# Performance work log

Measured on AMD Instinct MI355X. Metric: run time of the kernel, lower is better.

Reference implementation:

```python
import jax, jax.numpy as jnp
import numpy as np

B, L, D_MODEL, D_FF, N_EXPERTS, TOP_K = 32, 256, 512, 2048, 8, 2
EPS = 1e-9


def setup_inputs() -> dict:
    key = jax.random.key(0)
    ks = jax.random.split(key, 7)
    scale1 = 1.0 / np.sqrt(D_MODEL)
    scale2 = 1.0 / np.sqrt(D_FF)
    return {
        "cycle_curve_data": jax.random.normal(ks[0], (B, L, D_MODEL), jnp.float32),
        "logits": jax.random.normal(ks[1], (B, N_EXPERTS), jnp.float32),
        "moe_masks": jax.random.randint(ks[2], (B, N_EXPERTS), 0, 2, jnp.int32),
        "W1": jax.random.normal(ks[3], (N_EXPERTS, D_MODEL, D_FF), jnp.float32) * scale1,
        "b1": jax.random.normal(ks[4], (N_EXPERTS, D_FF), jnp.float32) * scale1,
        "W2": jax.random.normal(ks[5], (N_EXPERTS, D_FF, D_MODEL), jnp.float32) * scale2,
        "b2": jax.random.normal(ks[6], (N_EXPERTS, D_MODEL), jnp.float32) * scale2,
    }


def _gates(logits, moe_masks):
    # softmax over experts, zero out unavailable experts, keep top-k, renormalize
    mask = (moe_masks == 1).astype(logits.dtype)               # [B, E]
    p = jax.nn.softmax(logits, axis=1) * mask                  # [B, E]
    _, idx = jax.lax.top_k(p, TOP_K)                           # [B, K]
    topk_mask = jnp.zeros_like(p).at[jnp.arange(p.shape[0])[:, None], idx].set(1.0)
    p = p * topk_mask
    return p / (jnp.sum(p, axis=1, keepdims=True) + EPS)       # [B, E]


def reference(cycle_curve_data, logits, moe_masks, W1, b1, W2, b2):
    gates = _gates(logits, moe_masks)                          # [B, E]
    x = cycle_curve_data                                       # [B, L, D]
    # dense equivalent of per-expert gather -> MLP -> gate-weighted scatter-combine
    h = jnp.einsum("bld,edf->eblf", x, W1) + b1[:, None, None, :]   # [E,B,L,F]
    h = jax.nn.gelu(h, approximate=False)
    out = jnp.einsum("be,eblf,efd->bld", gates, h, W2)
    out = out + jnp.einsum("be,ed->bd", gates, b2)[:, None, :]      # [B,L,D]
    return out
```

## Files before the change

kernel.cpp:

```cpp
#include <hip/hip_runtime.h>

#define B_SZ 32
#define L_SZ 256
#define D_SZ 512
#define F_SZ 2048
#define E_SZ 8
#define P_SZ 64
#define BK2  32

typedef __attribute__((ext_vector_type(8)))  short bf16x8;
typedef __attribute__((ext_vector_type(16))) float f32x16;

__device__ __forceinline__ unsigned short f2bf(float f) {
  unsigned int u = __builtin_bit_cast(unsigned int, f);
  u += 0x7fffu + ((u >> 16) & 1u);
  return (unsigned short)(u >> 16);
}

__device__ __forceinline__ void async16(const void* g, void* l) {
  __builtin_amdgcn_global_load_lds(
      (const __attribute__((address_space(1))) unsigned int*)g,
      (__attribute__((address_space(3))) unsigned int*)l, 16, 0, 0);
}

__device__ __forceinline__ float gelu_f(float x) {
  float a = fabsf(x) * 0.70710678118654752f;
  float t = __builtin_amdgcn_rcpf(1.0f + 0.3275911f * a);
  float y = t * (0.254829592f +
            t * (-0.284496736f +
            t * (1.421413741f +
            t * (-1.453152027f +
            t * 1.061405429f))));
  float e = __expf(-a * a);
  float erf_abs = 1.0f - y * e;
  float erf_v = (x < 0.f) ? -erf_abs : erf_abs;
  return 0.5f * x * (1.0f + erf_v);
}

template <int NT>
__device__ __forceinline__ void transpose_tile(
    const float* __restrict__ ip, unsigned short* __restrict__ op,
    int R, int C, int r0, int c0, float* tile, int tid) {
  int tx = tid & 63, ty = tid >> 6;
  constexpr int RY = NT / 64;
#pragma unroll
  for (int i = 0; i < 64 / RY; ++i) {
    int r = i * RY + ty;
    tile[r * 65 + tx] = ip[(size_t)(r0 + r) * C + c0 + tx];
  }
  __syncthreads();
#pragma unroll
  for (int uu = 0; uu < 1024 / NT; ++uu) {
    int u = uu * NT + tid;
    int cc = u >> 4, q = u & 15;
    ushort4 o;
    o.x = f2bf(tile[(q * 4 + 0) * 65 + cc]);
    o.y = f2bf(tile[(q * 4 + 1) * 65 + cc]);
    o.z = f2bf(tile[(q * 4 + 2) * 65 + cc]);
    o.w = f2bf(tile[(q * 4 + 3) * 65 + cc]);
    *(ushort4*)(op + (size_t)(c0 + cc) * R + r0 + q * 4) = o;
  }
}

#define PREP_CONV_BLKS 4096
#define PREP_TR_BLKS   2048
#define PREP_TOTAL     (1 + PREP_CONV_BLKS + PREP_TR_BLKS)

__global__ __launch_bounds__(256) void prep_kernel(
    const float* __restrict__ logits, const int* __restrict__ masks,
    const float* __restrict__ x,
    const float* __restrict__ W1,
    int* __restrict__ sel_e, float* __restrict__ sel_g,
    unsigned short* __restrict__ xb,
    unsigned short* __restrict__ w1t) {
  __shared__ float tile[64 * 65];
  int blk = blockIdx.x;
  int tid = threadIdx.x;

  if (blk == 0) {
    int b = tid;
    if (b >= B_SZ) return;
    float lg[E_SZ], p[E_SZ];
    float mx = -1e30f;
    for (int e = 0; e < E_SZ; ++e) { lg[e] = logits[b * E_SZ + e]; mx = fmaxf(mx, lg[e]); }
    float s = 0.f;
    for (int e = 0; e < E_SZ; ++e) { p[e] = expf(lg[e] - mx); s += p[e]; }
    for (int e = 0; e < E_SZ; ++e) p[e] = (masks[b * E_SZ + e] == 1) ? (p[e] / s) : 0.f;
    int i0 = 0, i1 = 1; float v0 = -1.f, v1 = -1.f;
    for (int e = 0; e < E_SZ; ++e) {
      float v = p[e];
      if (v > v0)      { v1 = v0; i1 = i0; v0 = v; i0 = e; }
      else if (v > v1) { v1 = v;  i1 = e; }
    }
    float den = v0 + v1 + 1e-9f;
    sel_e[2 * b] = i0;  sel_e[2 * b + 1] = i1;
    sel_g[2 * b] = v0 / den;
    sel_g[2 * b + 1] = v1 / den;
    return;
  }
  blk -= 1;

  if (blk < PREP_CONV_BLKS) {
    int i = blk * 256 + tid;
    float4 v = ((const float4*)x)[i];
    ushort4 o;
    o.x = f2bf(v.x); o.y = f2bf(v.y); o.z = f2bf(v.z); o.w = f2bf(v.w);
    ((ushort4*)xb)[i] = o;
    return;
  }
  blk -= PREP_CONV_BLKS;

  int z = blk >> 8;
  int rem = blk & 255;
  int tr = rem >> 5, tc = rem & 31;
  transpose_tile<256>(W1 + (size_t)z * D_SZ * F_SZ, w1t + (size_t)z * D_SZ * F_SZ,
                      D_SZ, F_SZ, tr * 64, tc * 64, tile, tid);
}

__global__ __launch_bounds__(512, 4) void moe_gemm1(
    const unsigned short* __restrict__ Xb,
    const unsigned short* __restrict__ W1t,
    const float* __restrict__ b1,
    const int* __restrict__ sel_e,
    unsigned short* __restrict__ H,
    const float* __restrict__ W2,
    unsigned short* __restrict__ w2t) {
  __shared__ __align__(16) char smem[49152];
  int tid = threadIdx.x;
  int lin = blockIdx.x;

  if (lin >= 1024) {
    int blk = lin - 1024;
    int z = blk >> 8;
    int rem = blk & 255;
    int tr = rem >> 3, tc = rem & 7;
    transpose_tile<512>(W2 + (size_t)z * F_SZ * D_SZ, w2t + (size_t)z * F_SZ * D_SZ,
                        F_SZ, D_SZ, tr * 64, tc * 64, (float*)smem, tid);
    return;
  }

  unsigned short* As = (unsigned short*)smem;
  unsigned short* Bs = (unsigned short*)(smem + 16384);

  int f  = lin & 7;
  int l0 = ((lin >> 3) & 1) * 128;
  int p  = lin >> 4;
  int f0 = f * 256;
  int b  = p >> 1;
  int e  = sel_e[p];

  int lane = tid & 63;
  int w = tid >> 6;
  int wm = w & 1, wn = w >> 1;
  int m32 = lane & 31, kh = lane >> 5;
  int sw = (m32 >> 1) & 3;

  const unsigned short* Abase = Xb  + ((size_t)b * L_SZ + l0) * D_SZ;
  const unsigned short* Bbase = W1t + ((size_t)e * F_SZ + f0) * D_SZ;

  int sa   = tid;
  int rowa = sa >> 2,  ka  = ((sa  & 3) ^ ((rowa >> 1) & 3)) * 8;
  int sb1  = tid + 512;
  int rowb = sb1 >> 2, kb1 = ((sb1 & 3) ^ ((rowb >> 1) & 3)) * 8;

  const size_t aoffA  = (size_t)rowa * D_SZ + ka;
  const size_t aoffB1 = (size_t)rowb * D_SZ + kb1;

  f32x16 acc[2][2] = {};

#define G1_COMPUTE(CB)                                                       \
  _Pragma("unroll")                                                          \
  for (int s = 0; s < 2; ++s) {                                              \
    int ko = ((((s << 1) | kh) ^ sw) << 3);                                  \
    bf16x8 a0  = *(const bf16x8*)&As[(CB) * 4096 + (wm * 64 +      m32) * BK2 + ko]; \
    bf16x8 a1  = *(const bf16x8*)&As[(CB) * 4096 + (wm * 64 + 32 + m32) * BK2 + ko]; \
    bf16x8 b0  = *(const bf16x8*)&Bs[(CB) * 8192 + (wn * 64 +      m32) * BK2 + ko]; \
    bf16x8 b1f = *(const bf16x8*)&Bs[(CB) * 8192 + (wn * 64 + 32 + m32) * BK2 + ko]; \
    acc[0][0] = __builtin_amdgcn_mfma_f32_32x32x16_bf16(a0, b0,  acc[0][0], 0, 0, 0); \
    acc[0][1] = __builtin_amdgcn_mfma_f32_32x32x16_bf16(a0, b1f, acc[0][1], 0, 0, 0); \
    acc[1][0] = __builtin_amdgcn_mfma_f32_32x32x16_bf16(a1, b0,  acc[1][0], 0, 0, 0); \
    acc[1][1] = __builtin_amdgcn_mfma_f32_32x32x16_bf16(a1, b1f, acc[1][1], 0, 0, 0); \
  }

  async16(Abase + aoffA,  &As[sa * 8]);
  async16(Bbase + aoffA,  &Bs[sa * 8]);
  async16(Bbase + aoffB1, &Bs[sb1 * 8]);
  __syncthreads();

#pragma unroll 2
  for (int t = 0; t < 15; ++t) {
    int cb = t & 1, nb = cb ^ 1;
    int kk = (t + 1) * BK2;
    async16(Abase + aoffA  + kk, &As[nb * 4096 + sa * 8]);
    async16(Bbase + aoffA  + kk, &Bs[nb * 8192 + sa * 8]);
    async16(Bbase + aoffB1 + kk, &Bs[nb * 8192 + sb1 * 8]);
    G1_COMPUTE(cb)
    __syncthreads();
  }
  G1_COMPUTE(1)
#undef G1_COMPUTE

  float b1v[2];
#pragma unroll
  for (int tj = 0; tj < 2; ++tj)
    b1v[tj] = b1[e * F_SZ + f0 + wn * 64 + tj * 32 + m32];

  unsigned short* Hp = H + ((size_t)p * L_SZ + l0) * F_SZ + f0;
#pragma unroll
  for (int ti = 0; ti < 2; ++ti)
#pragma unroll
    for (int tj = 0; tj < 2; ++tj) {
      int col = wn * 64 + tj * 32 + m32;
#pragma unroll
      for (int r = 0; r < 16; ++r) {
        int row = wm * 64 + ti * 32 + (r & 3) + 8 * (r >> 2) + 4 * kh;
        Hp[(size_t)row * F_SZ + col] = f2bf(gelu_f(acc[ti][tj][r] + b1v[tj]));
      }
    }
}

__global__ __launch_bounds__(256, 4) void moe_gemm2(
    const unsigned short* __restrict__ H,
    const unsigned short* __restrict__ W2t,
    const float* __restrict__ b2,
    const int* __restrict__ sel_e,
    const float* __restrict__ sel_g,
    float* __restrict__ part,
    float* __restrict__ Out) {
  __shared__ __align__(16) unsigned short As[2][2][128 * BK2];
  __shared__ __align__(16) unsigned short Bs[2][2][128 * BK2];

  int lin = blockIdx.x;
  int q   = lin & 7;
  int d   = (lin >> 3) & 3;
  int g8  = lin >> 5;
  int gg  = g8 * 8 + q;
  int p   = gg >> 1;
  int l0  = (gg & 1) * 128;
  int d0  = d * 128;
  int b   = p >> 1;
  int e   = sel_e[p];
  float g = sel_g[p];

  int tid = threadIdx.x;
  int lane = tid & 63;
  int w = tid >> 6, wm = w & 1, wn = w >> 1;
  int m32 = lane & 31, kh = lane >> 5;
  int sw = (m32 >> 1) & 3;

  const unsigned short* Abase = H   + ((size_t)p * L_SZ + l0) * F_SZ;
  const unsigned short* Bbase = W2t + ((size_t)e * D_SZ + d0) * F_SZ;

  int seg0 = w * 128 + lane;
  int row0 = seg0 >> 2, ks0 = ((seg0 & 3) ^ ((row0 >> 1) & 3)) * 8;
  int seg1 = seg0 + 64;
  int row1 = seg1 >> 2, ks1 = ((seg1 & 3) ^ ((row1 >> 1) & 3)) * 8;

  const size_t aoff0 = (size_t)row0 * F_SZ + ks0;
  const size_t aoff1 = (size_t)row1 * F_SZ + ks1;

  f32x16 acc[2][2] = {};

#define G2_STAGE(NB, T) do {                                                 \
    size_t kk = (size_t)(T) * 64;                                            \
    async16(Abase + aoff0 + kk,      &As[NB][0][seg0 * 8]);                  \
    async16(Abase + aoff1 + kk,      &As[NB][0][seg1 * 8]);                  \
    async16(Bbase + aoff0 + kk,      &Bs[NB][0][seg0 * 8]);                  \
    async16(Bbase + aoff1 + kk,      &Bs[NB][0][seg1 * 8]);                  \
    async16(Abase + aoff0 + kk + 32, &As[NB][1][seg0 * 8]);                  \
    async16(Abase + aoff1 + kk + 32, &As[NB][1][seg1 * 8]);                  \
    async16(Bbase + aoff0 + kk + 32, &Bs[NB][1][seg0 * 8]);                  \
    async16(Bbase + aoff1 + kk + 32, &Bs[NB][1][seg1 * 8]);                  \
  } while (0)

#define G2_COMPUTE(CB)                                                       \
  _Pragma("unroll")                                                          \
  for (int h = 0; h < 2; ++h)                                                \
  _Pragma("unroll")                                                          \
  for (int s = 0; s < 2; ++s) {                                              \
    int ko = (((s << 1) | kh) ^ sw) << 3;                                    \
    bf16x8 a0  = *(const bf16x8*)&As[CB][h][(wm * 64 +      m32) * BK2 + ko]; \
    bf16x8 a1  = *(const bf16x8*)&As[CB][h][(wm * 64 + 32 + m32) * BK2 + ko]; \
    bf16x8 b0  = *(const bf16x8*)&Bs[CB][h][(wn * 64 +      m32) * BK2 + ko]; \
    bf16x8 b1f = *(const bf16x8*)&Bs[CB][h][(wn * 64 + 32 + m32) * BK2 + ko]; \
    acc[0][0] = __builtin_amdgcn_mfma_f32_32x32x16_bf16(a0, b0,  acc[0][0], 0, 0, 0); \
    acc[0][1] = __builtin_amdgcn_mfma_f32_32x32x16_bf16(a0, b1f, acc[0][1], 0, 0, 0); \
    acc[1][0] = __builtin_amdgcn_mfma_f32_32x32x16_bf16(a1, b0,  acc[1][0], 0, 0, 0); \
    acc[1][1] = __builtin_amdgcn_mfma_f32_32x32x16_bf16(a1, b1f, acc[1][1], 0, 0, 0); \
  }

  G2_STAGE(0, 0);
  __syncthreads();

#pragma unroll 2
  for (int t = 0; t < 31; ++t) {
    int cb = t & 1, nb = cb ^ 1;
    G2_STAGE(nb, t + 1);
    G2_COMPUTE(cb)
    __syncthreads();
  }
  G2_COMPUTE(1)
#undef G2_COMPUTE
#undef G2_STAGE

  float bias[2] = {0.f, 0.f};
  if (p & 1) {
    int e0 = sel_e[2 * b], e1 = sel_e[2 * b + 1];
    float g0 = sel_g[2 * b], g1 = sel_g[2 * b + 1];
#pragma unroll
    for (int tj = 0; tj < 2; ++tj) {
      int dd = d0 + wn * 64 + tj * 32 + m32;
      bias[tj] = g0 * b2[e0 * D_SZ + dd] + g1 * b2[e1 * D_SZ + dd];
    }
  }
  float* dst = (p & 1) ? Out : part;
  float* Op = dst + ((size_t)b * L_SZ + l0) * D_SZ + d0;
#pragma unroll
  for (int ti = 0; ti < 2; ++ti)
#pragma unroll
    for (int tj = 0; tj < 2; ++tj) {
      int col = wn * 64 + tj * 32 + m32;
#pragma unroll
      for (int r = 0; r < 16; ++r) {
        int row = wm * 64 + ti * 32 + (r & 3) + 8 * (r >> 2) + 4 * kh;
        Op[(size_t)row * D_SZ + col] = g * acc[ti][tj][r] + bias[tj];
      }
    }
}

__global__ __launch_bounds__(256) void combine_kernel(
    const float* __restrict__ part, float* __restrict__ Out) {
  int i = blockIdx.x * 256 + threadIdx.x;
  float4 pv = ((const float4*)part)[i];
  float4 o  = ((float4*)Out)[i];
  o.x += pv.x; o.y += pv.y; o.z += pv.z; o.w += pv.w;
  ((float4*)Out)[i] = o;
}

extern "C" void kernel_launch(void* const* d_in, const int* in_sizes, int n_in,
                              void* d_out, int out_size, void* d_ws, size_t ws_size,
                              hipStream_t stream) {
  const float* x      = (const float*)d_in[0];
  const float* logits = (const float*)d_in[1];
  const int*   masks  = (const int*)d_in[2];
  const float* W1     = (const float*)d_in[3];
  const float* b1     = (const float*)d_in[4];
  const float* W2     = (const float*)d_in[5];
  const float* b2     = (const float*)d_in[6];
  float* out = (float*)d_out;

  char* ws = (char*)d_ws;
  int*   sel_e = (int*)ws;
  float* sel_g = (float*)(ws + 256);
  unsigned short* xb  = (unsigned short*)(ws + 1024);
  unsigned short* w1t = xb  + (size_t)B_SZ * L_SZ * D_SZ;
  unsigned short* w2t = w1t + (size_t)E_SZ * F_SZ * D_SZ;
  unsigned short* Hbuf = w2t + (size_t)E_SZ * D_SZ * F_SZ;
  float* part = (float*)(ws + 1024);

  prep_kernel<<<PREP_TOTAL, 256, 0, stream>>>(logits, masks, x, W1,
                                              sel_e, sel_g, xb, w1t);
  moe_gemm1<<<3072, 512, 0, stream>>>(xb, w1t, b1, sel_e, Hbuf, W2, w2t);
  moe_gemm2<<<512, 256, 0, stream>>>(Hbuf, w2t, b2, sel_e, sel_g, part, out);
  combine_kernel<<<(B_SZ * L_SZ * D_SZ / 4) / 256, 256, 0, stream>>>(part, out);
}
```

Baseline: 248.2 us.

## Shrink gemm2 tiles to 128x64 with two waves and drop double buffering

The second expert GEMM now uses 128-thread blocks, each computing a 128x64 output tile, so the launch covers 1024 blocks instead of 512. The double-buffered LDS pipeline is replaced by a single-buffer load, sync, compute, sync loop. The aim is more blocks to spread across the CUs and a smaller LDS footprint per block. In exchange, loads no longer overlap with MFMA work inside a block, and the A tile is re-read from global memory once for each of the eight D tiles.

```diff
diff --git a/kernel.cpp b/kernel.cpp
--- a/kernel.cpp
+++ b/kernel.cpp
@@ -219,7 +219,7 @@
     }
 }
 
-__global__ __launch_bounds__(256, 4) void moe_gemm2(
+__global__ __launch_bounds__(128, 2) void moe_gemm2(
     const unsigned short* __restrict__ H,
     const unsigned short* __restrict__ W2t,
     const float* __restrict__ b2,
@@ -227,81 +227,75 @@
     const float* __restrict__ sel_g,
     float* __restrict__ part,
     float* __restrict__ Out) {
-  __shared__ __align__(16) unsigned short As[2][2][128 * BK2];
-  __shared__ __align__(16) unsigned short Bs[2][2][128 * BK2];
+  __shared__ __align__(16) unsigned short As[2][128 * BK2];
+  __shared__ __align__(16) unsigned short Bs[2][64 * BK2];
 
   int lin = blockIdx.x;
   int q   = lin & 7;
-  int d   = (lin >> 3) & 3;
-  int g8  = lin >> 5;
+  int d   = (lin >> 3) & 7;
+  int g8  = lin >> 6;
   int gg  = g8 * 8 + q;
   int p   = gg >> 1;
   int l0  = (gg & 1) * 128;
-  int d0  = d * 128;
+  int d0  = d * 64;
   int b   = p >> 1;
   int e   = sel_e[p];
   float g = sel_g[p];
 
   int tid = threadIdx.x;
   int lane = tid & 63;
-  int w = tid >> 6, wm = w & 1, wn = w >> 1;
+  int wm = tid >> 6;
   int m32 = lane & 31, kh = lane >> 5;
   int sw = (m32 >> 1) & 3;
 
   const unsigned short* Abase = H   + ((size_t)p * L_SZ + l0) * F_SZ;
   const unsigned short* Bbase = W2t + ((size_t)e * D_SZ + d0) * F_SZ;
 
-  int seg0 = w * 128 + lane;
-  int row0 = seg0 >> 2, ks0 = ((seg0 & 3) ^ ((row0 >> 1) & 3)) * 8;
-  int seg1 = seg0 + 64;
-  int row1 = seg1 >> 2, ks1 = ((seg1 & 3) ^ ((row1 >> 1) & 3)) * 8;
-
-  const size_t aoff0 = (size_t)row0 * F_SZ + ks0;
-  const size_t aoff1 = (size_t)row1 * F_SZ + ks1;
+  int    saA[4]; size_t aoffA[4];
+#pragma unroll
+  for (int j = 0; j < 4; ++j) {
+    int s = tid + j * 128;
+    int row = s >> 2, ks = ((s & 3) ^ ((row >> 1) & 3)) * 8;
+    saA[j] = s; aoffA[j] = (size_t)row * F_SZ + ks;
+  }
+  int    saB[2]; size_t aoffB[2];
+#pragma unroll
+  for (int j = 0; j < 2; ++j) {
+    int s = tid + j * 128;
+    int row = s >> 2, ks = ((s & 3) ^ ((row >> 1) & 3)) * 8;
+    saB[j] = s; aoffB[j] = (size_t)row * F_SZ + ks;
+  }
 
   f32x16 acc[2][2] = {};
 
-#define G2_STAGE(NB, T) do {                                                 \
-    size_t kk = (size_t)(T) * 64;                                            \
-    async16(Abase + aoff0 + kk,      &As[NB][0][seg0 * 8]);                  \
-    async16(Abase + aoff1 + kk,      &As[NB][0][seg1 * 8]);                  \
-    async16(Bbase + aoff0 + kk,      &Bs[NB][0][seg0 * 8]);                  \
-    async16(Bbase + aoff1 + kk,      &Bs[NB][0][seg1 * 8]);                  \
-    async16(Abase + aoff0 + kk + 32, &As[NB][1][seg0 * 8]);                  \
-    async16(Abase + aoff1 + kk + 32, &As[NB][1][seg1 * 8]);                  \
-    async16(Bbase + aoff0 + kk + 32, &Bs[NB][1][seg0 * 8]);                  \
-    async16(Bbase + aoff1 + kk + 32, &Bs[NB][1][seg1 * 8]);                  \
-  } while (0)
-
-#define G2_COMPUTE(CB)                                                       \
-  _Pragma("unroll")                                                          \
-  for (int h = 0; h < 2; ++h)                                                \
-  _Pragma("unroll")                                                          \
-  for (int s = 0; s < 2; ++s) {                                              \
-    int ko = (((s << 1) | kh) ^ sw) << 3;                                    \
-    bf16x8 a0  = *(const bf16x8*)&As[CB][h][(wm * 64 +      m32) * BK2 + ko]; \
-    bf16x8 a1  = *(const bf16x8*)&As[CB][h][(wm * 64 + 32 + m32) * BK2 + ko]; \
-    bf16x8 b0  = *(const bf16x8*)&Bs[CB][h][(wn * 64 +      m32) * BK2 + ko]; \
-    bf16x8 b1f = *(const bf16x8*)&Bs[CB][h][(wn * 64 + 32 + m32) * BK2 + ko]; \
-    acc[0][0] = __builtin_amdgcn_mfma_f32_32x32x16_bf16(a0, b0,  acc[0][0], 0, 0, 0); \
-    acc[0][1] = __builtin_amdgcn_mfma_f32_32x32x16_bf16(a0, b1f, acc[0][1], 0, 0, 0); \
-    acc[1][0] = __builtin_amdgcn_mfma_f32_32x32x16_bf16(a1, b0,  acc[1][0], 0, 0, 0); \
-    acc[1][1] = __builtin_amdgcn_mfma_f32_32x32x16_bf16(a1, b1f, acc[1][1], 0, 0, 0); \
-  }
-
-  G2_STAGE(0, 0);
-  __syncthreads();
-
-#pragma unroll 2
-  for (int t = 0; t < 31; ++t) {
-    int cb = t & 1, nb = cb ^ 1;
-    G2_STAGE(nb, t + 1);
-    G2_COMPUTE(cb)
+  for (int k0 = 0; k0 < F_SZ; k0 += 2 * BK2) {
+#pragma unroll
+    for (int h = 0; h < 2; ++h) {
+      int kk = k0 + h * BK2;
+#pragma unroll
+      for (int j = 0; j < 4; ++j)
+        async16(Abase + aoffA[j] + kk, &As[h][saA[j] * 8]);
+#pragma unroll
+      for (int j = 0; j < 2; ++j)
+        async16(Bbase + aoffB[j] + kk, &Bs[h][saB[j] * 8]);
+    }
     __syncthreads();
-  }
-  G2_COMPUTE(1)
-#undef G2_COMPUTE
-#undef G2_STAGE
+#pragma unroll
+    for (int h = 0; h < 2; ++h)
+#pragma unroll
+      for (int s = 0; s < 2; ++s) {
+        int ko = (((s << 1) | kh) ^ sw) << 3;
+        bf16x8 a0  = *(const bf16x8*)&As[h][(wm * 64 +      m32) * BK2 + ko];
+        bf16x8 a1  = *(const bf16x8*)&As[h][(wm * 64 + 32 + m32) * BK2 + ko];
+        bf16x8 b0  = *(const bf16x8*)&Bs[h][(          m32) * BK2 + ko];
+        bf16x8 b1f = *(const bf16x8*)&Bs[h][(     32 + m32) * BK2 + ko];
+        acc[0][0] = __builtin_amdgcn_mfma_f32_32x32x16_bf16(a0, b0,  acc[0][0], 0, 0, 0);
+        acc[0][1] = __builtin_amdgcn_mfma_f32_32x32x16_bf16(a0, b1f, acc[0][1], 0, 0, 0);
+        acc[1][0] = __builtin_amdgcn_mfma_f32_32x32x16_bf16(a1, b0,  acc[1][0], 0, 0, 0);
+        acc[1][1] = __builtin_amdgcn_mfma_f32_32x32x16_bf16(a1, b1f, acc[1][1], 0, 0, 0);
+      }
+    __syncthreads();
+  }
 
   float bias[2] = {0.f, 0.f};
   if (p & 1) {
@@ -309,7 +303,7 @@
     float g0 = sel_g[2 * b], g1 = sel_g[2 * b + 1];
 #pragma unroll
     for (int tj = 0; tj < 2; ++tj) {
-      int dd = d0 + wn * 64 + tj * 32 + m32;
+      int dd = d0 + tj * 32 + m32;
       bias[tj] = g0 * b2[e0 * D_SZ + dd] + g1 * b2[e1 * D_SZ + dd];
     }
   }
@@ -319,7 +313,7 @@
   for (int ti = 0; ti < 2; ++ti)
 #pragma unroll
     for (int tj = 0; tj < 2; ++tj) {
-      int col = wn * 64 + tj * 32 + m32;
+      int col = tj * 32 + m32;
 #pragma unroll
       for (int r = 0; r < 16; ++r) {
         int row = wm * 64 + ti * 32 + (r & 3) + 8 * (r >> 2) + 4 * kh;
@@ -361,6 +355,6 @@
   prep_kernel<<<PREP_TOTAL, 256, 0, stream>>>(logits, masks, x, W1,
                                               sel_e, sel_g, xb, w1t);
   moe_gemm1<<<3072, 512, 0, stream>>>(xb, w1t, b1, sel_e, Hbuf, W2, w2t);
-  moe_gemm2<<<512, 256, 0, stream>>>(Hbuf, w2t, b2, sel_e, sel_g, part, out);
+  moe_gemm2<<<1024, 128, 0, stream>>>(Hbuf, w2t, b2, sel_e, sel_g, part, out);
   combine_kernel<<<(B_SZ * L_SZ * D_SZ / 4) / 256, 256, 0, stream>>>(part, out);
 }
```

Result: faster. 242.7 us (-2.2%).
